# Kernel optimization log

Hardware: AMD Instinct MI355X
Metric: run time of the kernel (lower is better)

## Reference

```python
import jax, jax.numpy as jnp
import numpy as np

N_ATOMS = 10000
N_EDGES = 250000
F_DIM = 128
N_RBF = 20
CUTOFF = 5.0
N_INT = 3
EPS = 1e-8


def setup_inputs() -> dict:
    key = jax.random.key(0)
    ks = jax.random.split(key, 16)
    inp = {}
    inp["atomic_numbers"] = jax.random.randint(ks[0], (N_ATOMS,), 1, 101)
    # positions in a 5 Angstrom box so many pairs lie inside the cutoff
    inp["R"] = jax.random.uniform(ks[1], (N_ATOMS, 3), dtype=jnp.float32) * 5.0
    idx_i = jnp.sort(jax.random.randint(ks[2], (N_EDGES,), 0, N_ATOMS))
    # ensure idx_j != idx_i so d_ij > 0
    idx_j = (idx_i + 1 + jax.random.randint(ks[3], (N_EDGES,), 0, N_ATOMS - 1)) % N_ATOMS
    inp["idx_i"] = idx_i
    inp["idx_j"] = idx_j
    inp["offsets"] = jnp.zeros((N_EDGES, 3), dtype=jnp.float32)

    def w(k, shape):
        fan_in = shape[-2]
        return jax.random.normal(k, shape, dtype=jnp.float32) / np.sqrt(fan_in).astype(np.float32)

    inp["emb"] = jax.random.normal(ks[4], (101, F_DIM), dtype=jnp.float32)
    inp["filt_W"] = w(ks[5], (N_RBF, 3 * F_DIM))
    inp["filt_b"] = jax.random.normal(ks[6], (3 * F_DIM,), dtype=jnp.float32) * 0.01
    inp["int_W1"] = w(ks[7], (N_INT, F_DIM, F_DIM))
    inp["int_b1"] = jnp.zeros((N_INT, 1, F_DIM), dtype=jnp.float32)
    inp["int_W2"] = w(ks[8], (N_INT, F_DIM, 3 * F_DIM))
    inp["int_b2"] = jnp.zeros((N_INT, 1, 3 * F_DIM), dtype=jnp.float32)
    inp["mix_Wmu"] = w(ks[9], (N_INT, F_DIM, 2 * F_DIM))
    inp["mix_W1"] = w(ks[10], (N_INT, 2 * F_DIM, F_DIM))
    inp["mix_b1"] = jnp.zeros((N_INT, 1, F_DIM), dtype=jnp.float32)
    inp["mix_W2"] = w(ks[11], (N_INT, F_DIM, 3 * F_DIM))
    inp["mix_b2"] = jnp.zeros((N_INT, 1, 3 * F_DIM), dtype=jnp.float32)
    return inp


def painn_forward(atomic_numbers, idx_i, idx_j, R, offsets, emb, filt_W, filt_b,
                  int_W1, int_b1, int_W2, int_b2,
                  mix_Wmu, mix_W1, mix_b1, mix_W2, mix_b2):
    n_atoms = atomic_numbers.shape[0]
    # geometry
    r_ij = R[idx_j] - R[idx_i] + offsets                      # [E,3]
    d_ij = jnp.linalg.norm(r_ij, axis=1, keepdims=True)       # [E,1]
    dir_ij = r_ij / d_ij                                      # [E,3]
    # Gaussian radial basis + cosine cutoff (schnetpack defaults)
    centers = jnp.linspace(0.0, CUTOFF, N_RBF, dtype=jnp.float32)
    coeff = -0.5 / (centers[1] - centers[0]) ** 2
    phi = jnp.exp(coeff * (d_ij[..., None] - centers) ** 2)   # [E,1,N_RBF]
    fcut = 0.5 * (jnp.cos(d_ij * (jnp.pi / CUTOFF)) + 1.0) * (d_ij < CUTOFF)  # [E,1]
    Wij = (phi @ filt_W + filt_b) * fcut[..., None]           # [E,1,3F] (shared filters)

    q = emb[atomic_numbers][:, None, :]                       # [N,1,F]
    mu = jnp.zeros((n_atoms, 3, F_DIM), dtype=q.dtype)        # [N,3,F]

    for i in range(N_INT):
        # ---- interaction (equivariant message passing) ----
        x = jax.nn.silu(q @ int_W1[i] + int_b1[i]) @ int_W2[i] + int_b2[i]  # [N,1,3F]
        xj = x[idx_j]                                          # [E,1,3F]
        muj = mu[idx_j]                                        # [E,3,F]
        xw = Wij * xj                                          # [E,1,3F]
        dq, dmuR, dmumu = jnp.split(xw, 3, axis=-1)            # each [E,1,F]
        dq = jax.ops.segment_sum(dq, idx_i, num_segments=n_atoms)          # [N,1,F]
        dmu = dmuR * dir_ij[..., None] + dmumu * muj           # [E,3,F]
        dmu = jax.ops.segment_sum(dmu, idx_i, num_segments=n_atoms)        # [N,3,F]
        q = q + dq
        mu = mu + dmu
        # ---- mixing (intra-atomic) ----
        mu_mix = mu @ mix_Wmu[i]                               # [N,3,2F]
        mu_V, mu_W = jnp.split(mu_mix, 2, axis=-1)             # [N,3,F] each
        mu_Vn = jnp.sqrt(jnp.sum(mu_V ** 2, axis=-2, keepdims=True) + EPS)  # [N,1,F]
        ctx = jnp.concatenate([q, mu_Vn], axis=-1)             # [N,1,2F]
        xm = jax.nn.silu(ctx @ mix_W1[i] + mix_b1[i]) @ mix_W2[i] + mix_b2[i]  # [N,1,3F]
        dq_intra, dmu_intra, dqmu_intra = jnp.split(xm, 3, axis=-1)
        dmu_intra = dmu_intra * mu_W                           # [N,3,F]
        dqmu_intra = dqmu_intra * jnp.sum(mu_V * mu_W, axis=1, keepdims=True)  # [N,1,F]
        q = q + dq_intra + dqmu_intra
        mu = mu + dmu_intra

    return q.squeeze(1), mu                                    # [N,F], [N,3,F]


def reference(atomic_numbers, R, idx_i, idx_j, offsets, emb, filt_W, filt_b,
              int_W1, int_b1, int_W2, int_b2,
              mix_Wmu, mix_W1, mix_b1, mix_W2, mix_b2):
    return painn_forward(atomic_numbers, idx_i, idx_j, R, offsets, emb, filt_W, filt_b,
                         int_W1, int_b1, int_W2, int_b2,
                         mix_Wmu, mix_W1, mix_b1, mix_W2, mix_b2)
```

## Files before the change

kernel.cpp:

```cpp
#include <hip/hip_runtime.h>
#include <math.h>

#define NA 10000
#define NE 250000
#define FD 128
#define NRBF 20
#define RCUT 5.0f

typedef _Float16 h16;
typedef __attribute__((ext_vector_type(8))) _Float16 half8;
typedef __attribute__((ext_vector_type(2))) _Float16 half2v;
typedef __attribute__((ext_vector_type(4))) float f32x4;

static __device__ __forceinline__ half8 f32x8_to_h8(const float* p) {
    float4 a = *(const float4*)p;
    float4 b = *(const float4*)(p + 4);
    half8 r;
    r[0] = (h16)a.x; r[1] = (h16)a.y; r[2] = (h16)a.z; r[3] = (h16)a.w;
    r[4] = (h16)b.x; r[5] = (h16)b.y; r[6] = (h16)b.z; r[7] = (h16)b.w;
    return r;
}
static __device__ __forceinline__ float silu(float v) {
    return v / (1.f + expf(-v));
}

__global__ __launch_bounds__(256) void intmlp_kernel(
    const float* __restrict__ q, const h16* __restrict__ W1t, const float* __restrict__ b1,
    const h16* __restrict__ W2t, const float* __restrict__ b2, h16* __restrict__ x16)
{
    __shared__ h16 Hs[16 * 136];
    const int tid = threadIdx.x;
    const int wave = tid >> 6, lane = tid & 63;
    const int ar = lane & 15, kg = lane >> 4;
    const size_t row0 = (size_t)blockIdx.x * 16;

    f32x4 a1[2] = {};
    for (int ks = 0; ks < 128; ks += 32) {
        int k = ks + kg * 8;
        half8 af = f32x8_to_h8(q + (row0 + ar) * 128 + k);
#pragma unroll
        for (int tt = 0; tt < 2; ++tt) {
            int t = wave * 2 + tt;
            half8 bf = *(const half8*)&W1t[(size_t)(t * 16 + ar) * 128 + k];
            a1[tt] = __builtin_amdgcn_mfma_f32_16x16x32_f16(af, bf, a1[tt], 0, 0, 0);
        }
    }
#pragma unroll
    for (int tt = 0; tt < 2; ++tt) {
        int col = (wave * 2 + tt) * 16 + ar;
        float bb = b1[col];
#pragma unroll
        for (int r = 0; r < 4; ++r)
            Hs[(kg * 4 + r) * 136 + col] = (h16)silu(a1[tt][r] + bb);
    }
    __syncthreads();
    f32x4 a2[6] = {};
    for (int ks = 0; ks < 128; ks += 32) {
        int k = ks + kg * 8;
        half8 af = *(const half8*)&Hs[ar * 136 + k];
#pragma unroll
        for (int tt = 0; tt < 6; ++tt) {
            int t = wave * 6 + tt;
            half8 bf = *(const half8*)&W2t[(size_t)(t * 16 + ar) * 128 + k];
            a2[tt] = __builtin_amdgcn_mfma_f32_16x16x32_f16(af, bf, a2[tt], 0, 0, 0);
        }
    }
#pragma unroll
    for (int tt = 0; tt < 6; ++tt) {
        int col = (wave * 6 + tt) * 16 + ar;
        float bb = b2[col];
#pragma unroll
        for (int r = 0; r < 4; ++r)
            x16[(row0 + kg * 4 + r) * 384 + col] = (h16)(a2[tt][r] + bb);
    }
}

__global__ __launch_bounds__(256) void mixfused_kernel(
    const h16* __restrict__ mu16n, const h16* __restrict__ WmuT,
    const h16* __restrict__ W1t, const float* __restrict__ b1,
    const h16* __restrict__ W2t, const float* __restrict__ b2,
    float* __restrict__ q, float* __restrict__ mu, h16* __restrict__ mu16w)
{
    __shared__ h16 MM[48 * 264];
    __shared__ h16 CT[16 * 264];
    __shared__ h16 Hs[16 * 136];
    __shared__ h16 XM[16 * 392];
    const int tid = threadIdx.x;
    const int wave = tid >> 6, lane = tid & 63;
    const int ar = lane & 15, kg = lane >> 4;
    const size_t row0 = (size_t)blockIdx.x * 16;

    {
        f32x4 acc[3][4] = {};
        int aloc[3], dloc[3];
#pragma unroll
        for (int rt = 0; rt < 3; ++rt) {
            int rr = rt * 16 + ar;
            aloc[rt] = rr / 3;
            dloc[rt] = rr - 3 * aloc[rt];
        }
        for (int ks = 0; ks < 128; ks += 32) {
            int k = ks + kg * 8;
            half8 afr[3];
#pragma unroll
            for (int rt = 0; rt < 3; ++rt)
                afr[rt] = *(const half8*)&mu16n[(row0 + aloc[rt]) * 384 + dloc[rt] * 128 + k];
#pragma unroll
            for (int ct = 0; ct < 4; ++ct) {
                int c = wave * 4 + ct;
                half8 bf = *(const half8*)&WmuT[(size_t)(c * 16 + ar) * 128 + k];
#pragma unroll
                for (int rt = 0; rt < 3; ++rt)
                    acc[rt][ct] = __builtin_amdgcn_mfma_f32_16x16x32_f16(afr[rt], bf, acc[rt][ct], 0, 0, 0);
            }
        }
#pragma unroll
        for (int rt = 0; rt < 3; ++rt)
#pragma unroll
            for (int ct = 0; ct < 4; ++ct) {
                int col = (wave * 4 + ct) * 16 + ar;
#pragma unroll
                for (int r = 0; r < 4; ++r)
                    MM[(rt * 16 + kg * 4 + r) * 264 + col] = (h16)acc[rt][ct][r];
            }
    }
    __syncthreads();

    {
        int a = tid >> 4, fi = (tid & 15) * 8;
        const float* qp = q + (row0 + a) * 128 + fi;
        float4 q0 = *(const float4*)qp;
        float4 q1 = *(const float4*)(qp + 4);
        float qv[8] = {q0.x, q0.y, q0.z, q0.w, q1.x, q1.y, q1.z, q1.w};
#pragma unroll
        for (int jj = 0; jj < 8; ++jj) {
            int f = fi + jj;
            float v0 = (float)MM[(a * 3 + 0) * 264 + f];
            float v1 = (float)MM[(a * 3 + 1) * 264 + f];
            float v2 = (float)MM[(a * 3 + 2) * 264 + f];
            CT[a * 264 + 128 + f] = (h16)sqrtf(v0 * v0 + v1 * v1 + v2 * v2 + 1e-8f);
            CT[a * 264 + f] = (h16)qv[jj];
        }
    }
    __syncthreads();

    {
        f32x4 a1[2] = {};
        for (int ks = 0; ks < 256; ks += 32) {
            int k = ks + kg * 8;
            half8 af = *(const half8*)&CT[ar * 264 + k];
#pragma unroll
            for (int tt = 0; tt < 2; ++tt) {
                int t = wave * 2 + tt;
                half8 bf = *(const half8*)&W1t[(size_t)(t * 16 + ar) * 256 + k];
                a1[tt] = __builtin_amdgcn_mfma_f32_16x16x32_f16(af, bf, a1[tt], 0, 0, 0);
            }
        }
#pragma unroll
        for (int tt = 0; tt < 2; ++tt) {
            int col = (wave * 2 + tt) * 16 + ar;
            float bb = b1[col];
#pragma unroll
            for (int r = 0; r < 4; ++r)
                Hs[(kg * 4 + r) * 136 + col] = (h16)silu(a1[tt][r] + bb);
        }
    }
    __syncthreads();

    {
        f32x4 a2[6] = {};
        for (int ks = 0; ks < 128; ks += 32) {
            int k = ks + kg * 8;
            half8 af = *(const half8*)&Hs[ar * 136 + k];
#pragma unroll
            for (int tt = 0; tt < 6; ++tt) {
                int t = wave * 6 + tt;
                half8 bf = *(const half8*)&W2t[(size_t)(t * 16 + ar) * 128 + k];
                a2[tt] = __builtin_amdgcn_mfma_f32_16x16x32_f16(af, bf, a2[tt], 0, 0, 0);
            }
        }
#pragma unroll
        for (int tt = 0; tt < 6; ++tt) {
            int col = (wave * 6 + tt) * 16 + ar;
            float bb = b2[col];
#pragma unroll
            for (int r = 0; r < 4; ++r)
                XM[(kg * 4 + r) * 392 + col] = (h16)(a2[tt][r] + bb);
        }
    }
    __syncthreads();

    {
        int a = tid >> 4, fi = (tid & 15) * 8;
        size_t n = row0 + a;
#pragma unroll
        for (int jj = 0; jj < 8; ++jj) {
            int f = fi + jj;
            float dq  = (float)XM[a * 392 + f];
            float dm  = (float)XM[a * 392 + 128 + f];
            float dqm = (float)XM[a * 392 + 256 + f];
            float v0 = (float)MM[(a * 3 + 0) * 264 + f], w0 = (float)MM[(a * 3 + 0) * 264 + 128 + f];
            float v1 = (float)MM[(a * 3 + 1) * 264 + f], w1 = (float)MM[(a * 3 + 1) * 264 + 128 + f];
            float v2 = (float)MM[(a * 3 + 2) * 264 + f], w2 = (float)MM[(a * 3 + 2) * 264 + 128 + f];
            float sv = v0 * w0 + v1 * w1 + v2 * w2;
            q[n * 128 + f] += dq + dqm * sv;
            size_t b = n * 384 + f;
            float m0 = mu[b] + dm * w0;
            float m1 = mu[b + 128] + dm * w1;
            float m2 = mu[b + 256] + dm * w2;
            mu[b] = m0; mu[b + 128] = m1; mu[b + 256] = m2;
            mu16w[b] = (h16)m0; mu16w[b + 128] = (h16)m1; mu16w[b + 256] = (h16)m2;
        }
    }
}

__global__ void geom_kernel(const float* __restrict__ R,
                            const int* __restrict__ idx_i,
                            const int* __restrict__ idx_j,
                            const float* __restrict__ offsets,
                            float* __restrict__ dir, h16* __restrict__ ph)
{
    int e = blockIdx.x * blockDim.x + threadIdx.x;
    if (e >= NE) return;
    int i = idx_i[e], j = idx_j[e];
    float rx = R[j * 3 + 0] - R[i * 3 + 0] + offsets[e * 3 + 0];
    float ry = R[j * 3 + 1] - R[i * 3 + 1] + offsets[e * 3 + 1];
    float rz = R[j * 3 + 2] - R[i * 3 + 2] + offsets[e * 3 + 2];
    float d = sqrtf(rx * rx + ry * ry + rz * rz);
    float inv = 1.f / d;
    float fcut = 0.f;
    if (d < RCUT) fcut = 0.5f * (cosf(d * (3.14159265358979323846f / RCUT)) + 1.f);
    *(float4*)&dir[(size_t)e * 4] = make_float4(rx * inv, ry * inv, rz * inv, 0.f);
    h16* pp = ph + (size_t)e * 32;
    const float delta = RCUT / 19.f;
    const float coeff = -0.5f / (delta * delta);
#pragma unroll
    for (int r = 0; r < NRBF; ++r) {
        float dc = d - (float)r * delta;
        pp[r] = (h16)(expf(coeff * dc * dc) * fcut);
    }
    pp[20] = (h16)fcut;
#pragma unroll
    for (int r = 21; r < 32; ++r) pp[r] = (h16)0.f;
}

__global__ void csr_kernel(const int* __restrict__ idx_i, int* __restrict__ row_start)
{
    int n = blockIdx.x * blockDim.x + threadIdx.x;
    if (n > NA) return;
    int lo = 0, hi = NE;
    while (lo < hi) {
        int mid = (lo + hi) >> 1;
        if (idx_i[mid] < n) lo = mid + 1; else hi = mid;
    }
    row_start[n] = lo;
}

__global__ __launch_bounds__(128) void init_kernel(const int* __restrict__ Z,
                                                   const float* __restrict__ emb,
                                                   float* __restrict__ q,
                                                   float* __restrict__ mu_ws,
                                                   h16* __restrict__ mu16a)
{
    int n = blockIdx.x, f = threadIdx.x;
    q[(size_t)n * FD + f] = emb[(size_t)Z[n] * FD + f];
    float* m = mu_ws + (size_t)n * 384;
    m[f] = 0.f; m[128 + f] = 0.f; m[256 + f] = 0.f;
    h16* m16 = mu16a + (size_t)n * 384;
    m16[f] = (h16)0.f; m16[128 + f] = (h16)0.f; m16[256 + f] = (h16)0.f;
}

__global__ void wtrans_kernel(const float* __restrict__ W, h16* __restrict__ Bt,
                              int K, int N)
{
    int idx = blockIdx.x * 256 + threadIdx.x;
    int total = K * N;
    if (idx >= total) return;
    int n = idx / K, k = idx - n * K;
    Bt[(size_t)blockIdx.y * total + idx] =
        (h16)W[(size_t)blockIdx.y * total + (size_t)k * N + n];
}

__global__ void filtprep_kernel(const float* __restrict__ filt_W,
                                const float* __restrict__ filt_b,
                                h16* __restrict__ fwt)
{
    int idx = blockIdx.x * 256 + threadIdx.x;
    if (idx >= 384 * 32) return;
    int n = idx >> 5, k = idx & 31;
    float v = 0.f;
    if (k < 20) v = filt_W[k * 384 + n];
    else if (k == 20) v = filt_b[n];
    fwt[idx] = (h16)v;
}

__global__ __launch_bounds__(128) void edge_kernel(
    const float* __restrict__ dir, const h16* __restrict__ ph,
    const h16* __restrict__ fwt,
    const int* __restrict__ row_start, const int* __restrict__ idx_j,
    const h16* __restrict__ x16, const h16* __restrict__ mu16p,
    const float* __restrict__ mup, float* __restrict__ mun,
    h16* __restrict__ mu16n, float* __restrict__ q)
{
    const int n = blockIdx.x, f = threadIdx.x;
    half2v fa[16], fb[16], fc[16];
    {
        const half8* pa = (const half8*)(fwt + (size_t)f * 32);
        const half8* pb = (const half8*)(fwt + (size_t)(128 + f) * 32);
        const half8* pc = (const half8*)(fwt + (size_t)(256 + f) * 32);
#pragma unroll
        for (int r = 0; r < 3; ++r) {
            *(half8*)&fa[r * 4] = pa[r];
            *(half8*)&fb[r * 4] = pb[r];
            *(half8*)&fc[r * 4] = pc[r];
        }
    }
    float accq = 0.f, am0 = 0.f, am1 = 0.f, am2 = 0.f;
    const int e0 = row_start[n], e1 = row_start[n + 1];
    for (int e = e0; e < e1; ++e) {
        half2v pr[12];
        const h16* pb8 = ph + (size_t)e * 32;
        *(half8*)&pr[0] = *(const half8*)pb8;
        *(half8*)&pr[4] = *(const half8*)(pb8 + 8);
        *(half8*)&pr[8] = *(const half8*)(pb8 + 16);
        half2v A0 = {(h16)0.f, (h16)0.f}, A1 = A0, A2 = A0;
#pragma unroll
        for (int r = 0; r < 11; ++r) {
            A0 = pr[r] * fa[r] + A0;
            A1 = pr[r] * fb[r] + A1;
            A2 = pr[r] * fc[r] + A2;
        }
        float w0 = (float)A0[0] + (float)A0[1];
        float w1 = (float)A1[0] + (float)A1[1];
        float w2 = (float)A2[0] + (float)A2[1];
        int j = idx_j[e];
        float4 g = *(const float4*)&dir[(size_t)e * 4];
        const h16* xb = x16 + (size_t)j * 384;
        const h16* mb = mu16p + (size_t)j * 384;
        float x0 = (float)xb[f], x1 = (float)xb[128 + f], x2 = (float)xb[256 + f];
        accq = fmaf(w0, x0, accq);
        float xw1 = w1 * x1, xw2 = w2 * x2;
        am0 += xw1 * g.x + xw2 * (float)mb[f];
        am1 += xw1 * g.y + xw2 * (float)mb[128 + f];
        am2 += xw1 * g.z + xw2 * (float)mb[256 + f];
    }
    q[(size_t)n * FD + f] += accq;
    size_t b = (size_t)n * 384;
    float m0 = mup[b + f] + am0;
    float m1 = mup[b + 128 + f] + am1;
    float m2 = mup[b + 256 + f] + am2;
    mun[b + f] = m0; mun[b + 128 + f] = m1; mun[b + 256 + f] = m2;
    mu16n[b + f] = (h16)m0; mu16n[b + 128 + f] = (h16)m1; mu16n[b + 256 + f] = (h16)m2;
}

extern "C" void kernel_launch(void* const* d_in, const int* in_sizes, int n_in,
                              void* d_out, int out_size, void* d_ws, size_t ws_size,
                              hipStream_t stream)
{
    const int*   Z       = (const int*)d_in[0];
    const float* R       = (const float*)d_in[1];
    const int*   idx_i   = (const int*)d_in[2];
    const int*   idx_j   = (const int*)d_in[3];
    const float* offsets = (const float*)d_in[4];
    const float* emb     = (const float*)d_in[5];
    const float* filt_W  = (const float*)d_in[6];
    const float* filt_b  = (const float*)d_in[7];
    const float* int_W1  = (const float*)d_in[8];
    const float* int_b1  = (const float*)d_in[9];
    const float* int_W2  = (const float*)d_in[10];
    const float* int_b2  = (const float*)d_in[11];
    const float* mix_Wmu = (const float*)d_in[12];
    const float* mix_W1  = (const float*)d_in[13];
    const float* mix_b1  = (const float*)d_in[14];
    const float* mix_W2  = (const float*)d_in[15];
    const float* mix_b2  = (const float*)d_in[16];

    float* q_out  = (float*)d_out;
    float* mu_out = (float*)d_out + (size_t)NA * FD;

    char* base = (char*)d_ws;
    size_t o = 0;
    auto alloc = [&](size_t bytes) -> void* {
        void* p = base + o;
        o += (bytes + 255) & ~(size_t)255;
        return p;
    };
    float* dir    = (float*)alloc((size_t)NE * 4 * 4);
    h16*   ph     = (h16*)alloc((size_t)NE * 32 * 2);
    h16*   x16    = (h16*)alloc((size_t)NA * 384 * 2);
    h16*   mu16a  = (h16*)alloc((size_t)NA * 384 * 2);
    h16*   mu16b  = (h16*)alloc((size_t)NA * 384 * 2);
    float* mu_ws  = (float*)alloc((size_t)NA * 384 * 4);
    h16*   W1t    = (h16*)alloc((size_t)3 * 128 * 128 * 2);
    h16*   W2t    = (h16*)alloc((size_t)3 * 384 * 128 * 2);
    h16*   WmuT   = (h16*)alloc((size_t)3 * 256 * 128 * 2);
    h16*   mW1t   = (h16*)alloc((size_t)3 * 128 * 256 * 2);
    h16*   mW2t   = (h16*)alloc((size_t)3 * 384 * 128 * 2);
    h16*   fwt    = (h16*)alloc((size_t)384 * 32 * 2);
    int*   row_st = (int*)alloc((size_t)(NA + 1) * 4);

    geom_kernel<<<(NE + 255) / 256, 256, 0, stream>>>(R, idx_i, idx_j, offsets, dir, ph);
    csr_kernel<<<(NA + 256) / 256, 256, 0, stream>>>(idx_i, row_st);
    init_kernel<<<NA, 128, 0, stream>>>(Z, emb, q_out, mu_ws, mu16a);
    wtrans_kernel<<<dim3((128 * 128 + 255) / 256, 3), 256, 0, stream>>>(int_W1, W1t, 128, 128);
    wtrans_kernel<<<dim3((128 * 384 + 255) / 256, 3), 256, 0, stream>>>(int_W2, W2t, 128, 384);
    wtrans_kernel<<<dim3((128 * 256 + 255) / 256, 3), 256, 0, stream>>>(mix_Wmu, WmuT, 128, 256);
    wtrans_kernel<<<dim3((256 * 128 + 255) / 256, 3), 256, 0, stream>>>(mix_W1, mW1t, 256, 128);
    wtrans_kernel<<<dim3((128 * 384 + 255) / 256, 3), 256, 0, stream>>>(mix_W2, mW2t, 128, 384);
    filtprep_kernel<<<(384 * 32 + 255) / 256, 256, 0, stream>>>(filt_W, filt_b, fwt);

    for (int it = 0; it < 3; ++it) {
        const h16*   W1i  = W1t  + (size_t)it * 128 * 128;
        const float* b1i  = int_b1 + (size_t)it * 128;
        const h16*   W2i  = W2t  + (size_t)it * 384 * 128;
        const float* b2i  = int_b2 + (size_t)it * 384;
        const h16*   Wmui = WmuT + (size_t)it * 256 * 128;
        const h16*   mW1i = mW1t + (size_t)it * 128 * 256;
        const float* mb1i = mix_b1 + (size_t)it * 128;
        const h16*   mW2i = mW2t + (size_t)it * 384 * 128;
        const float* mb2i = mix_b2 + (size_t)it * 384;

        float* mu_prev = (it & 1) ? mu_out : mu_ws;
        float* mu_next = (it & 1) ? mu_ws : mu_out;
        h16*   m16p    = (it & 1) ? mu16b : mu16a;
        h16*   m16n    = (it & 1) ? mu16a : mu16b;

        intmlp_kernel<<<NA / 16, 256, 0, stream>>>(q_out, W1i, b1i, W2i, b2i, x16);
        edge_kernel<<<NA, 128, 0, stream>>>(dir, ph, fwt, row_st, idx_j,
                                            x16, m16p, mu_prev, mu_next, m16n, q_out);
        mixfused_kernel<<<NA / 16, 256, 0, stream>>>(m16n, Wmui, mW1i, mb1i, mW2i, mb2i,
                                                     q_out, mu_next, m16n);
    }
}
```

Measured before the change: 489.6 us.

## Fuse setup kernels, fold next interaction MLP into mixing, MFMA edge filters

Merges geometry, CSR, weight transposes and filter prep into one setup launch, and fuses the embedding init into the first interaction MLP. The mixing kernel now also runs the next iteration's interaction MLP, which removes a launch and a reload of q per iteration. The edge kernel computes filter weights for 16 edges at a time with an MFMA into shared memory, replacing per-thread half2 dot products, and it skips the zero mu reads on the first iteration. The cost is extra syncthreads and shared-memory traffic per edge chunk, plus larger, more complex kernels.

```diff
diff --git a/kernel.cpp b/kernel.cpp
--- a/kernel.cpp
+++ b/kernel.cpp
@@ -9,7 +9,6 @@
 
 typedef _Float16 h16;
 typedef __attribute__((ext_vector_type(8))) _Float16 half8;
-typedef __attribute__((ext_vector_type(2))) _Float16 half2v;
 typedef __attribute__((ext_vector_type(4))) float f32x4;
 
 static __device__ __forceinline__ half8 f32x8_to_h8(const float* p) {
@@ -24,8 +23,86 @@
     return v / (1.f + expf(-v));
 }
 
-__global__ __launch_bounds__(256) void intmlp_kernel(
-    const float* __restrict__ q, const h16* __restrict__ W1t, const float* __restrict__ b1,
+__global__ __launch_bounds__(256) void setup_kernel(
+    const float* __restrict__ R, const int* __restrict__ idx_i,
+    const int* __restrict__ idx_j, const float* __restrict__ offsets,
+    float* __restrict__ dir, h16* __restrict__ ph, int* __restrict__ row_start,
+    const float* __restrict__ int_W1, const float* __restrict__ int_W2,
+    const float* __restrict__ mix_Wmu, const float* __restrict__ mix_W1,
+    const float* __restrict__ mix_W2,
+    h16* __restrict__ W1t, h16* __restrict__ W2t, h16* __restrict__ WmuT,
+    h16* __restrict__ mW1t, h16* __restrict__ mW2t,
+    const float* __restrict__ filt_W, const float* __restrict__ filt_b,
+    h16* __restrict__ fwt)
+{
+    const int b = blockIdx.x;
+    if (b < 977) {
+        int e = b * 256 + threadIdx.x;
+        if (e >= NE) return;
+        int i = idx_i[e], j = idx_j[e];
+        float rx = R[j * 3 + 0] - R[i * 3 + 0] + offsets[e * 3 + 0];
+        float ry = R[j * 3 + 1] - R[i * 3 + 1] + offsets[e * 3 + 1];
+        float rz = R[j * 3 + 2] - R[i * 3 + 2] + offsets[e * 3 + 2];
+        float d = sqrtf(rx * rx + ry * ry + rz * rz);
+        float inv = 1.f / d;
+        float fcut = 0.f;
+        if (d < RCUT) fcut = 0.5f * (cosf(d * (3.14159265358979323846f / RCUT)) + 1.f);
+        *(float4*)&dir[(size_t)e * 4] = make_float4(rx * inv, ry * inv, rz * inv, 0.f);
+        h16* pp = ph + (size_t)e * 32;
+        const float delta = RCUT / 19.f;
+        const float coeff = -0.5f / (delta * delta);
+#pragma unroll
+        for (int r = 0; r < NRBF; ++r) {
+            float dc = d - (float)r * delta;
+            pp[r] = (h16)(expf(coeff * dc * dc) * fcut);
+        }
+        pp[20] = (h16)fcut;
+#pragma unroll
+        for (int r = 21; r < 32; ++r) pp[r] = (h16)0.f;
+    } else if (b < 1017) {
+        int n = (b - 977) * 256 + threadIdx.x;
+        if (n > NA) return;
+        int lo = 0, hi = NE;
+        while (lo < hi) {
+            int mid = (lo + hi) >> 1;
+            if (idx_i[mid] < n) lo = mid + 1; else hi = mid;
+        }
+        row_start[n] = lo;
+    } else {
+        int idx = (b - 1017) * 256 + threadIdx.x;
+        if (idx < 49152) {
+            int bt = idx >> 14, rem = idx & 16383;
+            int nn = rem >> 7, kk = rem & 127;
+            W1t[idx] = (h16)int_W1[(size_t)bt * 16384 + kk * 128 + nn];
+        } else if ((idx -= 49152) < 147456) {
+            int bt = idx / 49152, rem = idx - bt * 49152;
+            int nn = rem >> 7, kk = rem & 127;
+            W2t[idx] = (h16)int_W2[(size_t)bt * 49152 + kk * 384 + nn];
+        } else if ((idx -= 147456) < 98304) {
+            int bt = idx >> 15, rem = idx & 32767;
+            int nn = rem >> 7, kk = rem & 127;
+            WmuT[idx] = (h16)mix_Wmu[(size_t)bt * 32768 + kk * 256 + nn];
+        } else if ((idx -= 98304) < 98304) {
+            int bt = idx >> 15, rem = idx & 32767;
+            int nn = rem >> 8, kk = rem & 255;
+            mW1t[idx] = (h16)mix_W1[(size_t)bt * 32768 + kk * 128 + nn];
+        } else if ((idx -= 98304) < 147456) {
+            int bt = idx / 49152, rem = idx - bt * 49152;
+            int nn = rem >> 7, kk = rem & 127;
+            mW2t[idx] = (h16)mix_W2[(size_t)bt * 49152 + kk * 384 + nn];
+        } else if ((idx -= 147456) < 12288) {
+            int nn = idx >> 5, kk = idx & 31;
+            float v = 0.f;
+            if (kk < 20) v = filt_W[kk * 384 + nn];
+            else if (kk == 20) v = filt_b[nn];
+            fwt[idx] = (h16)v;
+        }
+    }
+}
+
+__global__ __launch_bounds__(256) void intmlp0_kernel(
+    const int* __restrict__ Z, const float* __restrict__ emb, float* __restrict__ q,
+    const h16* __restrict__ W1t, const float* __restrict__ b1,
     const h16* __restrict__ W2t, const float* __restrict__ b2, h16* __restrict__ x16)
 {
     __shared__ h16 Hs[16 * 136];
@@ -34,10 +111,19 @@
     const int ar = lane & 15, kg = lane >> 4;
     const size_t row0 = (size_t)blockIdx.x * 16;
 
+    {
+        int a = tid >> 4, f0 = (tid & 15) * 8;
+        const float* src = emb + (size_t)Z[row0 + a] * 128 + f0;
+        float4 v0 = *(const float4*)src;
+        float4 v1 = *(const float4*)(src + 4);
+        *(float4*)&q[(row0 + a) * 128 + f0] = v0;
+        *(float4*)&q[(row0 + a) * 128 + f0 + 4] = v1;
+    }
+    const int zr = Z[row0 + ar];
     f32x4 a1[2] = {};
     for (int ks = 0; ks < 128; ks += 32) {
         int k = ks + kg * 8;
-        half8 af = f32x8_to_h8(q + (row0 + ar) * 128 + k);
+        half8 af = f32x8_to_h8(emb + (size_t)zr * 128 + k);
 #pragma unroll
         for (int tt = 0; tt < 2; ++tt) {
             int t = wave * 2 + tt;
@@ -75,11 +161,76 @@
     }
 }
 
-__global__ __launch_bounds__(256) void mixfused_kernel(
+__global__ __launch_bounds__(128) void edge_kernel(
+    const float* __restrict__ dir, const h16* __restrict__ ph,
+    const h16* __restrict__ fwt,
+    const int* __restrict__ row_start, const int* __restrict__ idx_j,
+    const h16* __restrict__ x16, const h16* __restrict__ mu16p,
+    const float* __restrict__ mup, float* __restrict__ mun,
+    h16* __restrict__ mu16n, float* __restrict__ q)
+{
+    __shared__ h16 Wl[16 * 392];
+    const int n = blockIdx.x, tid = threadIdx.x;
+    const int wave = tid >> 6, lane = tid & 63;
+    const int ar = lane & 15, kg = lane >> 4;
+    const int f = tid;
+    const int e0 = row_start[n], e1 = row_start[n + 1];
+    float accq = 0.f, am0 = 0.f, am1 = 0.f, am2 = 0.f;
+
+    for (int eg = e0; eg < e1; eg += 16) {
+        int esrc = eg + ar; if (esrc >= e1) esrc = e1 - 1;
+        half8 af = *(const half8*)&ph[(size_t)esrc * 32 + kg * 8];
+#pragma unroll
+        for (int tt = 0; tt < 12; ++tt) {
+            int t = wave * 12 + tt;
+            half8 bf = *(const half8*)&fwt[(size_t)(t * 16 + ar) * 32 + kg * 8];
+            f32x4 c = {0.f, 0.f, 0.f, 0.f};
+            c = __builtin_amdgcn_mfma_f32_16x16x32_f16(af, bf, c, 0, 0, 0);
+#pragma unroll
+            for (int r = 0; r < 4; ++r)
+                Wl[(kg * 4 + r) * 392 + t * 16 + ar] = (h16)c[r];
+        }
+        __syncthreads();
+        const int ee = (eg + 16 < e1) ? eg + 16 : e1;
+        for (int e = eg; e < ee; ++e) {
+            const h16* wp = Wl + (size_t)(e - eg) * 392;
+            float w0 = (float)wp[f], w1 = (float)wp[128 + f], w2 = (float)wp[256 + f];
+            int j = idx_j[e];
+            float4 g = *(const float4*)&dir[(size_t)e * 4];
+            const h16* xb = x16 + (size_t)j * 384;
+            float x0 = (float)xb[f], x1 = (float)xb[128 + f], x2 = (float)xb[256 + f];
+            accq = fmaf(w0, x0, accq);
+            float xw1 = w1 * x1, xw2 = w2 * x2;
+            if (mu16p) {
+                const h16* mb = mu16p + (size_t)j * 384;
+                am0 += xw1 * g.x + xw2 * (float)mb[f];
+                am1 += xw1 * g.y + xw2 * (float)mb[128 + f];
+                am2 += xw1 * g.z + xw2 * (float)mb[256 + f];
+            } else {
+                am0 += xw1 * g.x;
+                am1 += xw1 * g.y;
+                am2 += xw1 * g.z;
+            }
+        }
+        __syncthreads();
+    }
+    q[(size_t)n * FD + f] += accq;
+    size_t b = (size_t)n * 384;
+    float m0 = (mup ? mup[b + f] : 0.f) + am0;
+    float m1 = (mup ? mup[b + 128 + f] : 0.f) + am1;
+    float m2 = (mup ? mup[b + 256 + f] : 0.f) + am2;
+    mun[b + f] = m0; mun[b + 128 + f] = m1; mun[b + 256 + f] = m2;
+    mu16n[b + f] = (h16)m0; mu16n[b + 128 + f] = (h16)m1; mu16n[b + 256 + f] = (h16)m2;
+}
+
+__global__ __launch_bounds__(256) void mixint_kernel(
     const h16* __restrict__ mu16n, const h16* __restrict__ WmuT,
     const h16* __restrict__ W1t, const float* __restrict__ b1,
     const h16* __restrict__ W2t, const float* __restrict__ b2,
-    float* __restrict__ q, float* __restrict__ mu, h16* __restrict__ mu16w)
+    float* __restrict__ q, float* __restrict__ mu, h16* __restrict__ mu16w,
+    const h16* __restrict__ nW1t, const float* __restrict__ nb1,
+    const h16* __restrict__ nW2t, const float* __restrict__ nb2,
+    h16* __restrict__ x16)
 {
     __shared__ h16 MM[48 * 264];
     __shared__ h16 CT[16 * 264];
@@ -134,12 +285,12 @@
         float qv[8] = {q0.x, q0.y, q0.z, q0.w, q1.x, q1.y, q1.z, q1.w};
 #pragma unroll
         for (int jj = 0; jj < 8; ++jj) {
-            int f = fi + jj;
-            float v0 = (float)MM[(a * 3 + 0) * 264 + f];
-            float v1 = (float)MM[(a * 3 + 1) * 264 + f];
-            float v2 = (float)MM[(a * 3 + 2) * 264 + f];
-            CT[a * 264 + 128 + f] = (h16)sqrtf(v0 * v0 + v1 * v1 + v2 * v2 + 1e-8f);
-            CT[a * 264 + f] = (h16)qv[jj];
+            int ff = fi + jj;
+            float v0 = (float)MM[(a * 3 + 0) * 264 + ff];
+            float v1 = (float)MM[(a * 3 + 1) * 264 + ff];
+            float v2 = (float)MM[(a * 3 + 2) * 264 + ff];
+            CT[a * 264 + 128 + ff] = (h16)sqrtf(v0 * v0 + v1 * v1 + v2 * v2 + 1e-8f);
+            CT[a * 264 + ff] = (h16)qv[jj];
         }
     }
     __syncthreads();
@@ -195,16 +346,18 @@
         size_t n = row0 + a;
 #pragma unroll
         for (int jj = 0; jj < 8; ++jj) {
-            int f = fi + jj;
-            float dq  = (float)XM[a * 392 + f];
-            float dm  = (float)XM[a * 392 + 128 + f];
-            float dqm = (float)XM[a * 392 + 256 + f];
-            float v0 = (float)MM[(a * 3 + 0) * 264 + f], w0 = (float)MM[(a * 3 + 0) * 264 + 128 + f];
-            float v1 = (float)MM[(a * 3 + 1) * 264 + f], w1 = (float)MM[(a * 3 + 1) * 264 + 128 + f];
-            float v2 = (float)MM[(a * 3 + 2) * 264 + f], w2 = (float)MM[(a * 3 + 2) * 264 + 128 + f];
+            int ff = fi + jj;
+            float dq  = (float)XM[a * 392 + ff];
+            float dm  = (float)XM[a * 392 + 128 + ff];
+            float dqm = (float)XM[a * 392 + 256 + ff];
+            float v0 = (float)MM[(a * 3 + 0) * 264 + ff], w0 = (float)MM[(a * 3 + 0) * 264 + 128 + ff];
+            float v1 = (float)MM[(a * 3 + 1) * 264 + ff], w1 = (float)MM[(a * 3 + 1) * 264 + 128 + ff];
+            float v2 = (float)MM[(a * 3 + 2) * 264 + ff], w2 = (float)MM[(a * 3 + 2) * 264 + 128 + ff];
             float sv = v0 * w0 + v1 * w1 + v2 * w2;
-            q[n * 128 + f] += dq + dqm * sv;
-            size_t b = n * 384 + f;
+            float qn = q[n * 128 + ff] + dq + dqm * sv;
+            q[n * 128 + ff] = qn;
+            CT[a * 264 + ff] = (h16)qn;
+            size_t b = n * 384 + ff;
             float m0 = mu[b] + dm * w0;
             float m1 = mu[b + 128] + dm * w1;
             float m2 = mu[b + 256] + dm * w2;
@@ -212,145 +365,50 @@
             mu16w[b] = (h16)m0; mu16w[b + 128] = (h16)m1; mu16w[b + 256] = (h16)m2;
         }
     }
-}
-
-__global__ void geom_kernel(const float* __restrict__ R,
-                            const int* __restrict__ idx_i,
-                            const int* __restrict__ idx_j,
-                            const float* __restrict__ offsets,
-                            float* __restrict__ dir, h16* __restrict__ ph)
-{
-    int e = blockIdx.x * blockDim.x + threadIdx.x;
-    if (e >= NE) return;
-    int i = idx_i[e], j = idx_j[e];
-    float rx = R[j * 3 + 0] - R[i * 3 + 0] + offsets[e * 3 + 0];
-    float ry = R[j * 3 + 1] - R[i * 3 + 1] + offsets[e * 3 + 1];
-    float rz = R[j * 3 + 2] - R[i * 3 + 2] + offsets[e * 3 + 2];
-    float d = sqrtf(rx * rx + ry * ry + rz * rz);
-    float inv = 1.f / d;
-    float fcut = 0.f;
-    if (d < RCUT) fcut = 0.5f * (cosf(d * (3.14159265358979323846f / RCUT)) + 1.f);
-    *(float4*)&dir[(size_t)e * 4] = make_float4(rx * inv, ry * inv, rz * inv, 0.f);
-    h16* pp = ph + (size_t)e * 32;
-    const float delta = RCUT / 19.f;
-    const float coeff = -0.5f / (delta * delta);
-#pragma unroll
-    for (int r = 0; r < NRBF; ++r) {
-        float dc = d - (float)r * delta;
-        pp[r] = (h16)(expf(coeff * dc * dc) * fcut);
-    }
-    pp[20] = (h16)fcut;
-#pragma unroll
-    for (int r = 21; r < 32; ++r) pp[r] = (h16)0.f;
-}
-
-__global__ void csr_kernel(const int* __restrict__ idx_i, int* __restrict__ row_start)
-{
-    int n = blockIdx.x * blockDim.x + threadIdx.x;
-    if (n > NA) return;
-    int lo = 0, hi = NE;
-    while (lo < hi) {
-        int mid = (lo + hi) >> 1;
-        if (idx_i[mid] < n) lo = mid + 1; else hi = mid;
-    }
-    row_start[n] = lo;
-}
-
-__global__ __launch_bounds__(128) void init_kernel(const int* __restrict__ Z,
-                                                   const float* __restrict__ emb,
-                                                   float* __restrict__ q,
-                                                   float* __restrict__ mu_ws,
-                                                   h16* __restrict__ mu16a)
-{
-    int n = blockIdx.x, f = threadIdx.x;
-    q[(size_t)n * FD + f] = emb[(size_t)Z[n] * FD + f];
-    float* m = mu_ws + (size_t)n * 384;
-    m[f] = 0.f; m[128 + f] = 0.f; m[256 + f] = 0.f;
-    h16* m16 = mu16a + (size_t)n * 384;
-    m16[f] = (h16)0.f; m16[128 + f] = (h16)0.f; m16[256 + f] = (h16)0.f;
-}
-
-__global__ void wtrans_kernel(const float* __restrict__ W, h16* __restrict__ Bt,
-                              int K, int N)
-{
-    int idx = blockIdx.x * 256 + threadIdx.x;
-    int total = K * N;
-    if (idx >= total) return;
-    int n = idx / K, k = idx - n * K;
-    Bt[(size_t)blockIdx.y * total + idx] =
-        (h16)W[(size_t)blockIdx.y * total + (size_t)k * N + n];
-}
-
-__global__ void filtprep_kernel(const float* __restrict__ filt_W,
-                                const float* __restrict__ filt_b,
-                                h16* __restrict__ fwt)
-{
-    int idx = blockIdx.x * 256 + threadIdx.x;
-    if (idx >= 384 * 32) return;
-    int n = idx >> 5, k = idx & 31;
-    float v = 0.f;
-    if (k < 20) v = filt_W[k * 384 + n];
-    else if (k == 20) v = filt_b[n];
-    fwt[idx] = (h16)v;
-}
-
-__global__ __launch_bounds__(128) void edge_kernel(
-    const float* __restrict__ dir, const h16* __restrict__ ph,
-    const h16* __restrict__ fwt,
-    const int* __restrict__ row_start, const int* __restrict__ idx_j,
-    const h16* __restrict__ x16, const h16* __restrict__ mu16p,
-    const float* __restrict__ mup, float* __restrict__ mun,
-    h16* __restrict__ mu16n, float* __restrict__ q)
-{
-    const int n = blockIdx.x, f = threadIdx.x;
-    half2v fa[16], fb[16], fc[16];
-    {
-        const half8* pa = (const half8*)(fwt + (size_t)f * 32);
-        const half8* pb = (const half8*)(fwt + (size_t)(128 + f) * 32);
-        const half8* pc = (const half8*)(fwt + (size_t)(256 + f) * 32);
-#pragma unroll
-        for (int r = 0; r < 3; ++r) {
-            *(half8*)&fa[r * 4] = pa[r];
-            *(half8*)&fb[r * 4] = pb[r];
-            *(half8*)&fc[r * 4] = pc[r];
-        }
-    }
-    float accq = 0.f, am0 = 0.f, am1 = 0.f, am2 = 0.f;
-    const int e0 = row_start[n], e1 = row_start[n + 1];
-    for (int e = e0; e < e1; ++e) {
-        half2v pr[12];
-        const h16* pb8 = ph + (size_t)e * 32;
-        *(half8*)&pr[0] = *(const half8*)pb8;
-        *(half8*)&pr[4] = *(const half8*)(pb8 + 8);
-        *(half8*)&pr[8] = *(const half8*)(pb8 + 16);
-        half2v A0 = {(h16)0.f, (h16)0.f}, A1 = A0, A2 = A0;
-#pragma unroll
-        for (int r = 0; r < 11; ++r) {
-            A0 = pr[r] * fa[r] + A0;
-            A1 = pr[r] * fb[r] + A1;
-            A2 = pr[r] * fc[r] + A2;
-        }
-        float w0 = (float)A0[0] + (float)A0[1];
-        float w1 = (float)A1[0] + (float)A1[1];
-        float w2 = (float)A2[0] + (float)A2[1];
-        int j = idx_j[e];
-        float4 g = *(const float4*)&dir[(size_t)e * 4];
-        const h16* xb = x16 + (size_t)j * 384;
-        const h16* mb = mu16p + (size_t)j * 384;
-        float x0 = (float)xb[f], x1 = (float)xb[128 + f], x2 = (float)xb[256 + f];
-        accq = fmaf(w0, x0, accq);
-        float xw1 = w1 * x1, xw2 = w2 * x2;
-        am0 += xw1 * g.x + xw2 * (float)mb[f];
-        am1 += xw1 * g.y + xw2 * (float)mb[128 + f];
-        am2 += xw1 * g.z + xw2 * (float)mb[256 + f];
-    }
-    q[(size_t)n * FD + f] += accq;
-    size_t b = (size_t)n * 384;
-    float m0 = mup[b + f] + am0;
-    float m1 = mup[b + 128 + f] + am1;
-    float m2 = mup[b + 256 + f] + am2;
-    mun[b + f] = m0; mun[b + 128 + f] = m1; mun[b + 256 + f] = m2;
-    mu16n[b + f] = (h16)m0; mu16n[b + 128 + f] = (h16)m1; mu16n[b + 256 + f] = (h16)m2;
+    if (!nW1t) return;
+    __syncthreads();
+
+    {
+        f32x4 a1[2] = {};
+        for (int ks = 0; ks < 128; ks += 32) {
+            int k = ks + kg * 8;
+            half8 af = *(const half8*)&CT[ar * 264 + k];
+#pragma unroll
+            for (int tt = 0; tt < 2; ++tt) {
+                int t = wave * 2 + tt;
+                half8 bf = *(const half8*)&nW1t[(size_t)(t * 16 + ar) * 128 + k];
+                a1[tt] = __builtin_amdgcn_mfma_f32_16x16x32_f16(af, bf, a1[tt], 0, 0, 0);
+            }
+        }
+#pragma unroll
+        for (int tt = 0; tt < 2; ++tt) {
+            int col = (wave * 2 + tt) * 16 + ar;
+            float bb = nb1[col];
+#pragma unroll
+            for (int r = 0; r < 4; ++r)
+                Hs[(kg * 4 + r) * 136 + col] = (h16)silu(a1[tt][r] + bb);
+        }
+        __syncthreads();
+        f32x4 a2[6] = {};
+        for (int ks = 0; ks < 128; ks += 32) {
+            int k = ks + kg * 8;
+            half8 af = *(const half8*)&Hs[ar * 136 + k];
+#pragma unroll
+            for (int tt = 0; tt < 6; ++tt) {
+                int t = wave * 6 + tt;
+                half8 bf = *(const half8*)&nW2t[(size_t)(t * 16 + ar) * 128 + k];
+                a2[tt] = __builtin_amdgcn_mfma_f32_16x16x32_f16(af, bf, a2[tt], 0, 0, 0);
+            }
+        }
+#pragma unroll
+        for (int tt = 0; tt < 6; ++tt) {
+            int col = (wave * 6 + tt) * 16 + ar;
+            float bb = nb2[col];
+#pragma unroll
+            for (int r = 0; r < 4; ++r)
+                x16[(row0 + kg * 4 + r) * 384 + col] = (h16)(a2[tt][r] + bb);
+        }
+    }
 }
 
 extern "C" void kernel_launch(void* const* d_in, const int* in_sizes, int n_in,
@@ -399,36 +457,30 @@
     h16*   fwt    = (h16*)alloc((size_t)384 * 32 * 2);
     int*   row_st = (int*)alloc((size_t)(NA + 1) * 4);
 
-    geom_kernel<<<(NE + 255) / 256, 256, 0, stream>>>(R, idx_i, idx_j, offsets, dir, ph);
-    csr_kernel<<<(NA + 256) / 256, 256, 0, stream>>>(idx_i, row_st);
-    init_kernel<<<NA, 128, 0, stream>>>(Z, emb, q_out, mu_ws, mu16a);
-    wtrans_kernel<<<dim3((128 * 128 + 255) / 256, 3), 256, 0, stream>>>(int_W1, W1t, 128, 128);
-    wtrans_kernel<<<dim3((128 * 384 + 255) / 256, 3), 256, 0, stream>>>(int_W2, W2t, 128, 384);
-    wtrans_kernel<<<dim3((128 * 256 + 255) / 256, 3), 256, 0, stream>>>(mix_Wmu, WmuT, 128, 256);
-    wtrans_kernel<<<dim3((256 * 128 + 255) / 256, 3), 256, 0, stream>>>(mix_W1, mW1t, 256, 128);
-    wtrans_kernel<<<dim3((128 * 384 + 255) / 256, 3), 256, 0, stream>>>(mix_W2, mW2t, 128, 384);
-    filtprep_kernel<<<(384 * 32 + 255) / 256, 256, 0, stream>>>(filt_W, filt_b, fwt);
-
-    for (int it = 0; it < 3; ++it) {
-        const h16*   W1i  = W1t  + (size_t)it * 128 * 128;
-        const float* b1i  = int_b1 + (size_t)it * 128;
-        const h16*   W2i  = W2t  + (size_t)it * 384 * 128;
-        const float* b2i  = int_b2 + (size_t)it * 384;
-        const h16*   Wmui = WmuT + (size_t)it * 256 * 128;
-        const h16*   mW1i = mW1t + (size_t)it * 128 * 256;
-        const float* mb1i = mix_b1 + (size_t)it * 128;
-        const h16*   mW2i = mW2t + (size_t)it * 384 * 128;
-        const float* mb2i = mix_b2 + (size_t)it * 384;
-
-        float* mu_prev = (it & 1) ? mu_out : mu_ws;
-        float* mu_next = (it & 1) ? mu_ws : mu_out;
-        h16*   m16p    = (it & 1) ? mu16b : mu16a;
-        h16*   m16n    = (it & 1) ? mu16a : mu16b;
-
-        intmlp_kernel<<<NA / 16, 256, 0, stream>>>(q_out, W1i, b1i, W2i, b2i, x16);
-        edge_kernel<<<NA, 128, 0, stream>>>(dir, ph, fwt, row_st, idx_j,
-                                            x16, m16p, mu_prev, mu_next, m16n, q_out);
-        mixfused_kernel<<<NA / 16, 256, 0, stream>>>(m16n, Wmui, mW1i, mb1i, mW2i, mb2i,
-                                                     q_out, mu_next, m16n);
-    }
-}
+    setup_kernel<<<3177, 256, 0, stream>>>(R, idx_i, idx_j, offsets, dir, ph, row_st,
+                                           int_W1, int_W2, mix_Wmu, mix_W1, mix_W2,
+                                           W1t, W2t, WmuT, mW1t, mW2t,
+                                           filt_W, filt_b, fwt);
+
+    intmlp0_kernel<<<NA / 16, 256, 0, stream>>>(Z, emb, q_out,
+                                                W1t, int_b1, W2t, int_b2, x16);
+    edge_kernel<<<NA, 128, 0, stream>>>(dir, ph, fwt, row_st, idx_j,
+                                        x16, nullptr, nullptr, mu_out, mu16b, q_out);
+    mixint_kernel<<<NA / 16, 256, 0, stream>>>(
+        mu16b, WmuT, mW1t, mix_b1, mW2t, mix_b2, q_out, mu_out, mu16b,
+        W1t + 16384, int_b1 + 128, W2t + 49152, int_b2 + 384, x16);
+
+    edge_kernel<<<NA, 128, 0, stream>>>(dir, ph, fwt, row_st, idx_j,
+                                        x16, mu16b, mu_out, mu_ws, mu16a, q_out);
+    mixint_kernel<<<NA / 16, 256, 0, stream>>>(
+        mu16a, WmuT + 32768, mW1t + 32768, mix_b1 + 128, mW2t + 49152, mix_b2 + 384,
+        q_out, mu_ws, mu16a,
+        W1t + 32768, int_b1 + 256, W2t + 98304, int_b2 + 768, x16);
+
+    edge_kernel<<<NA, 128, 0, stream>>>(dir, ph, fwt, row_st, idx_j,
+                                        x16, mu16a, mu_ws, mu_out, mu16b, q_out);
+    mixint_kernel<<<NA / 16, 256, 0, stream>>>(
+        mu16b, WmuT + 65536, mW1t + 65536, mix_b1 + 256, mW2t + 98304, mix_b2 + 768,
+        q_out, mu_out, mu16b,
+        nullptr, nullptr, nullptr, nullptr, nullptr);
+}
```

Result: slower. 576.0 us (+17.7%).
